# Kernel tuning notes

Measured on AMD Instinct MI355X. Metric: run time of the kernel, lower is better.

Reference implementation:

```python
import jax, jax.numpy as jnp
import numpy as np

B, N, C, H, D = 4, 2048, 512, 8, 64
W = 4            # chunk_window
TOKEEP = 64      # max_keep_keys
NW = N // W      # number of query windows (N divisible by W -> no padding)


def setup_inputs() -> dict:
    key = jax.random.key(0)
    ks = jax.random.split(key, 6)
    x = jax.random.normal(ks[0], (B, N, C), jnp.float32)
    mask = jnp.zeros((B, N), dtype=bool)  # True = padded position
    pos_bias = jax.random.normal(ks[1], (H, N, N), jnp.float32) * 0.02
    # Pareto(scale=3, alpha=2) samples: scale * U^(-1/alpha)
    u = jax.random.uniform(ks[2], (B, H, NW, N), jnp.float32, minval=1e-6, maxval=1.0)
    pareto_noise = 3.0 * u ** (-0.5)
    Wqkv = jax.random.normal(ks[3], (C, 3 * H * D), jnp.float32) * (C ** -0.5)
    bqkv = jnp.zeros((3 * H * D,), jnp.float32)
    Wo = jax.random.normal(ks[4], (H * D, C), jnp.float32) * ((H * D) ** -0.5)
    bo = jnp.zeros((C,), jnp.float32)
    return {"x": x, "mask": mask, "pos_bias": pos_bias, "pareto_noise": pareto_noise,
            "Wqkv": Wqkv, "bqkv": bqkv, "Wo": Wo, "bo": bo}


def reference(x, mask, pos_bias, pareto_noise, Wqkv, bqkv, Wo, bo):
    scale = D ** -0.5
    big = jnp.finfo(x.dtype).max
    # qkv projection; einops '(h d qkv)' => qkv is the innermost factor
    qkv = (x @ Wqkv + bqkv).reshape(B, N, H, D, 3)
    q = qkv[..., 0].transpose(0, 2, 1, 3)  # [B,H,N,D]
    k = qkv[..., 1].transpose(0, 2, 1, 3)
    v = qkv[..., 2].transpose(0, 2, 1, 3)
    q = q.reshape(B, H, NW, W, D)          # windowed queries

    # chunk-distance grid: |chunk_i - chunk_j| repeated W times along keys -> [NW, N]
    ci = jnp.arange(NW)
    grid = jnp.abs(ci[None, :] - ci[:, None]).astype(x.dtype)
    grid = jnp.repeat(grid, W, axis=1)     # [NW, N]
    noised = grid[None, None] - pareto_noise               # [B,H,NW,N]
    noised = jnp.where(mask[:, None, None, :], big, noised)  # padded keys -> never kept

    # keep the TOKEEP smallest (closest, noise-perturbed) keys per window
    _, idx = jax.lax.top_k(-noised, TOKEEP)
    idx = jnp.sort(idx, axis=-1)           # [B,H,NW,K]

    # gather selected keys/values: [B,H,NW,K,D]
    k_sel = jnp.take_along_axis(k[:, :, None], idx[..., None], axis=3)
    v_sel = jnp.take_along_axis(v[:, :, None], idx[..., None], axis=3)

    # position bias gathered at kept keys: [B,H,NW,W,K]
    pb = pos_bias.reshape(H, NW, W, N)[None]
    pb = jnp.take_along_axis(pb, idx[:, :, :, None, :], axis=4)

    dots = jnp.einsum('bhnwd,bhnzd->bhnwz', q, k_sel) * scale + pb

    q_mask = jnp.broadcast_to(mask.reshape(B, 1, NW, W), (B, H, NW, W))
    kv_mask = jnp.take_along_axis(mask[:, None, None, :], idx, axis=3)  # [B,H,NW,K]
    qk = q_mask[..., None] & kv_mask[:, :, :, None, :]  # bool*bool == AND (as in torch code)
    dots = jnp.where(qk, -big, dots)

    attn = jax.nn.softmax(dots, axis=-1)
    out = jnp.einsum('bhnwz,bhnzd->bhnwd', attn, v_sel)   # [B,H,NW,W,D]
    out = out.transpose(0, 2, 3, 1, 4).reshape(B, N, H * D)  # 'b h n w d -> b (n w) (h d)'
    return out @ Wo + bo
```

## Files before the change

kernel.cpp:

```cpp
#include <hip/hip_runtime.h>
#include <stdint.h>

typedef unsigned short u16;
typedef unsigned int u32;
typedef unsigned long long u64;

#define B_ 4
#define N_ 2048
#define C_ 512
#define H_ 8
#define D_ 64
#define W_ 4
#define NW_ 512
#define KEEP_ 64

__device__ __forceinline__ float bf2f(u16 h) { return __uint_as_float(((u32)h) << 16); }
__device__ __forceinline__ u16 f2bf(float f) {
  u32 u = __float_as_uint(f);
  u32 r = (u + 0x7FFFu + ((u >> 16) & 1u)) >> 16;
  return (u16)r;
}
__device__ __forceinline__ u32 flip32(float f) {
  u32 u = __float_as_uint(f);
  return (u & 0x80000000u) ? ~u : (u | 0x80000000u);
}

typedef short bf16x8 __attribute__((ext_vector_type(8)));
typedef float f32x4 __attribute__((ext_vector_type(4)));

__device__ __forceinline__ void async_copy16(u16* lds, const u16* g) {
#if __has_builtin(__builtin_amdgcn_global_load_lds)
  __builtin_amdgcn_global_load_lds((const __attribute__((address_space(1))) u32*)g,
                                   (__attribute__((address_space(3))) u32*)lds, 16, 0, 0);
#else
  const int lane = threadIdx.x & 63;
  *(((uint4*)lds) + lane) = *(const uint4*)g;
#endif
}

__global__ __launch_bounds__(256) void cast_f32_bf16(
    const float* __restrict__ in, u16* __restrict__ out)
{
  const int i = blockIdx.x * 256 + threadIdx.x;
  float4 v = ((const float4*)in)[i];
  uint2 o;
  o.x = (u32)f2bf(v.x) | ((u32)f2bf(v.y) << 16);
  o.y = (u32)f2bf(v.z) | ((u32)f2bf(v.w) << 16);
  ((uint2*)out)[i] = o;
}

__global__ __launch_bounds__(256) void cast_transpose(
    const float* __restrict__ in, u16* __restrict__ out, int R, int C)
{
  __shared__ float tile[64][65];
  const int r0 = blockIdx.y * 64, c0 = blockIdx.x * 64;
  const int tr = threadIdx.x >> 4;
  const int tc = (threadIdx.x & 15) * 4;
#pragma unroll
  for (int i = 0; i < 4; i++) {
    const int r = tr + i * 16;
    float4 v = *(const float4*)(in + (size_t)(r0 + r) * C + c0 + tc);
    tile[r][tc] = v.x; tile[r][tc + 1] = v.y; tile[r][tc + 2] = v.z; tile[r][tc + 3] = v.w;
  }
  __syncthreads();
#pragma unroll
  for (int i = 0; i < 4; i++) {
    const int rr = tr + i * 16;
    uint2 o;
    o.x = (u32)f2bf(tile[tc][rr]) | ((u32)f2bf(tile[tc + 1][rr]) << 16);
    o.y = (u32)f2bf(tile[tc + 2][rr]) | ((u32)f2bf(tile[tc + 3][rr]) << 16);
    *(uint2*)(out + (size_t)(c0 + rr) * R + r0 + tc) = o;
  }
}

template <int MODE>
__global__ __launch_bounds__(256) void gemm_bt(
    const u16* __restrict__ A, const u16* __restrict__ BT, const float* __restrict__ bias,
    void* __restrict__ O0, void* __restrict__ O1, void* __restrict__ O2,
    int M, int N, int K)
{
  __shared__ u16 As[128 * 32];
  __shared__ u16 Bs[128 * 32];
  const int tid = threadIdx.x;
  const int wid = tid >> 6, lane = tid & 63;
  const int tileM = blockIdx.y * 128, tileN = blockIdx.x * 128;
  const int wr = wid >> 1, wc = wid & 1;

  f32x4 acc[4][4];
#pragma unroll
  for (int i = 0; i < 4; i++)
#pragma unroll
    for (int j = 0; j < 4; j++) acc[i][j] = (f32x4){0.f, 0.f, 0.f, 0.f};

  const int srow = wid * 32 + (lane >> 2);
  const int scol = (lane & 3) * 8;
  const u16* Ag = A + (size_t)(tileM + srow) * K + scol;
  const u16* Bg = BT + (size_t)(tileN + srow) * K + scol;
  u16* AsW = As + wid * 32 * 32;
  u16* BsW = Bs + wid * 32 * 32;

  const int fr = lane & 15, fq = lane >> 4;

  for (int k0 = 0; k0 < K; k0 += 32) {
    __syncthreads();
    async_copy16(AsW, Ag + k0);
    async_copy16(AsW + 16 * 32, Ag + k0 + (size_t)16 * K);
    async_copy16(BsW, Bg + k0);
    async_copy16(BsW + 16 * 32, Bg + k0 + (size_t)16 * K);
    asm volatile("s_waitcnt vmcnt(0)" ::: "memory");
    __syncthreads();

    bf16x8 af[4], bfr[4];
#pragma unroll
    for (int tm = 0; tm < 4; tm++)
      af[tm] = *(const bf16x8*)(As + (wr * 64 + tm * 16 + fr) * 32 + fq * 8);
#pragma unroll
    for (int tn = 0; tn < 4; tn++)
      bfr[tn] = *(const bf16x8*)(Bs + (wc * 64 + tn * 16 + fr) * 32 + fq * 8);
#pragma unroll
    for (int tm = 0; tm < 4; tm++)
#pragma unroll
      for (int tn = 0; tn < 4; tn++)
        acc[tm][tn] = __builtin_amdgcn_mfma_f32_16x16x32_bf16(af[tm], bfr[tn], acc[tm][tn], 0, 0, 0);
  }

#pragma unroll
  for (int tm = 0; tm < 4; tm++) {
#pragma unroll
    for (int tn = 0; tn < 4; tn++) {
      const int colb = tileN + wc * 64 + tn * 16 + fr;
      const float bi = bias[colb];
      if (MODE == 0) {
        const int h = colb / 192;
        const int rem = colb - h * 192;
        const int d = rem / 3;
        const int tq = rem - d * 3;
        u16* dst = (tq == 0) ? (u16*)O0 : (tq == 1) ? (u16*)O1 : (u16*)O2;
#pragma unroll
        for (int r = 0; r < 4; r++) {
          const int row = tileM + wr * 64 + tm * 16 + fq * 4 + r;
          const int b = row >> 11, n = row & 2047;
          const size_t off = (((size_t)(b * 8 + h)) * 2048 + n) * 64 + d;
          dst[off] = f2bf(acc[tm][tn][r] + bi);
        }
      } else {
        float* Of = (float*)O0;
#pragma unroll
        for (int r = 0; r < 4; r++) {
          const int row = tileM + wr * 64 + tm * 16 + fq * 4 + r;
          Of[(size_t)row * N + colb] = acc[tm][tn][r] + bi;
        }
      }
    }
  }
}

__global__ __launch_bounds__(256) void select_topk(
    const float* __restrict__ noise, u16* __restrict__ idx_out)
{
  const int wid = threadIdx.x >> 6;
  const int lane = threadIdx.x & 63;
  const int pid = blockIdx.x * 4 + wid;
  const int nw = pid & (NW_ - 1);

  __shared__ u64 pool_s[4][512];
  u64* pool = pool_s[wid];

  const int s = min(nw, (NW_ - 1) - nw);
  const float T = (s >= 8) ? 5.0f : (float)(12 - s);

  const float* row = noise + (size_t)pid * N_;
  float4 f[8];
#pragma unroll
  for (int k = 0; k < 8; k++)
    f[k] = *(const float4*)(row + k * 256 + lane * 4);

  const u64 lmask = (1ull << lane) - 1ull;
  u32 c = 0;
#pragma unroll
  for (int k = 0; k < 8; k++) {
    const int ci = k * 64 + lane;
    const int dd = nw - ci;
    const float g = (float)(dd < 0 ? -dd : dd);
    const float vv[4] = {f[k].x, f[k].y, f[k].z, f[k].w};
#pragma unroll
    for (int e = 0; e < 4; e++) {
      const float v = g - vv[e];
      const bool sv = (v <= T);
      const u64 mask = __ballot(sv);
      if (sv) {
        const u32 pos = c + (u32)__popcll(mask & lmask);
        const int j = k * 256 + lane * 4 + e;
        if (pos < 512) pool[pos] = ((u64)flip32(v) << 16) | (u32)j;
      }
      c += (u32)__popcll(mask);
    }
  }
  __syncthreads();

  u16* outp = idx_out + (size_t)pid * KEEP_;

  if (__builtin_expect(c > 512, 0)) {
    u32 taken = 0;
    u16 keep = 0;
    for (int r = 0; r < 64; r++) {
      u64 best = ~0ull;
      int bslot = -1;
#pragma unroll
      for (int k = 0; k < 8; k++) {
        const int ci = k * 64 + lane;
        const int dd = nw - ci;
        const float g = (float)(dd < 0 ? -dd : dd);
        const float vv[4] = {f[k].x, f[k].y, f[k].z, f[k].w};
#pragma unroll
        for (int e = 0; e < 4; e++) {
          const int sl = k * 4 + e;
          if (!(taken & (1u << sl))) {
            const int j = k * 256 + lane * 4 + e;
            const u64 p = ((u64)flip32(g - vv[e]) << 16) | (u32)j;
            if (p < best) { best = p; bslot = sl; }
          }
        }
      }
      u64 m = best;
#pragma unroll
      for (int st = 1; st < 64; st <<= 1) {
        const u64 o = __shfl_xor(m, st, 64);
        if (o < m) m = o;
      }
      if (best == m) taken |= (1u << bslot);
      if (lane == r) keep = (u16)(m & 0xFFFFu);
    }
    outp[lane] = keep;
    return;
  }

  u64 q[8];
#pragma unroll
  for (int k = 0; k < 8; k++) {
    const u32 sl = (u32)lane + (u32)(k << 6);
    q[k] = (sl < c) ? pool[sl] : 0ull;
  }
  int cnt = ((u32)lane < c) ? (int)((c - 1 - (u32)lane) >> 6) + 1 : 0;

#define CE_(a, b) { if (q[a] < q[b]) { u64 t_ = q[a]; q[a] = q[b]; q[b] = t_; } }
  CE_(0,1) CE_(2,3) CE_(4,5) CE_(6,7)
  CE_(0,2) CE_(1,3) CE_(4,6) CE_(5,7)
  CE_(1,2) CE_(5,6)
  CE_(0,4) CE_(1,5) CE_(2,6) CE_(3,7)
  CE_(2,4) CE_(3,5)
  CE_(1,2) CE_(3,4) CE_(5,6)
#undef CE_

  const int R = (int)c - KEEP_;
  for (int r = 0; r < R; r++) {
    u64 m = q[0];
#pragma unroll
    for (int st = 1; st < 64; st <<= 1) {
      const u64 o = __shfl_xor(m, st, 64);
      if (o > m) m = o;
    }
    if (q[0] == m) {
      q[0] = q[1]; q[1] = q[2]; q[2] = q[3]; q[3] = q[4];
      q[4] = q[5]; q[5] = q[6]; q[6] = q[7]; q[7] = 0ull;
      cnt--;
    }
  }

  u32 off = (u32)cnt;
#pragma unroll
  for (int st = 1; st < 64; st <<= 1) {
    const u32 o = __shfl_up(off, st, 64);
    if (lane >= st) off += o;
  }
  off -= (u32)cnt;
#pragma unroll
  for (int k = 0; k < 8; k++)
    if (k < cnt) outp[off + k] = (u16)(q[k] & 0xFFFFu);
}

__global__ __launch_bounds__(256) void attn_kernel(
    const u16* __restrict__ Q, const u16* __restrict__ Kt, const u16* __restrict__ Vt,
    const float* __restrict__ pos_bias, const u16* __restrict__ idx, u16* __restrict__ outp)
{
  const int bid = blockIdx.x;
  const int b = bid & 3;
  const int hn = bid >> 2;
  const int h = hn >> 9;
  const int nw = hn & (NW_ - 1);
  const int bh = b * H_ + h;
  const int pid = bh * NW_ + nw;
  const int t = threadIdx.x;

  __shared__ float q_s[W_][D_];
  __shared__ u16 k_s[64 * 66];
  __shared__ u16 v_s[64 * 66];
  __shared__ float attn_s[W_][64];
  __shared__ u16 idx_s[64];

  if (t < 64) {
    idx_s[t] = idx[(size_t)pid * KEEP_ + t];
    const int w = t >> 4, dq = (t & 15) * 4;
    uint2 v = *(const uint2*)(Q + ((size_t)bh * N_ + nw * W_ + w) * D_ + dq);
    q_s[w][dq] = bf2f((u16)(v.x & 0xFFFF));
    q_s[w][dq + 1] = bf2f((u16)(v.x >> 16));
    q_s[w][dq + 2] = bf2f((u16)(v.y & 0xFFFF));
    q_s[w][dq + 3] = bf2f((u16)(v.y >> 16));
  }
  __syncthreads();

  const int w2 = t >> 6, z2 = t & 63;
  float pb;
  {
    const int z = t >> 2, c = t & 3;
    const u32 kidx = idx_s[z];
    const u16* kr = Kt + ((size_t)bh * N_ + kidx) * D_ + c * 16;
    const u16* vr = Vt + ((size_t)bh * N_ + kidx) * D_ + c * 16;
    uint4 ka = *(const uint4*)kr;
    uint4 kb = *(const uint4*)(kr + 8);
    uint4 va = *(const uint4*)vr;
    uint4 vb = *(const uint4*)(vr + 8);
    u32* kd = (u32*)(k_s + z * 66 + c * 16);
    u32* vd = (u32*)(v_s + z * 66 + c * 16);
    kd[0] = ka.x; kd[1] = ka.y; kd[2] = ka.z; kd[3] = ka.w;
    kd[4] = kb.x; kd[5] = kb.y; kd[6] = kb.z; kd[7] = kb.w;
    vd[0] = va.x; vd[1] = va.y; vd[2] = va.z; vd[3] = va.w;
    vd[4] = vb.x; vd[5] = vb.y; vd[6] = vb.z; vd[7] = vb.w;
    pb = pos_bias[((size_t)h * N_ + nw * W_ + w2) * N_ + idx_s[z2]];
  }
  __syncthreads();

  float accd = 0.f;
  const u16* krow = k_s + z2 * 66;
#pragma unroll
  for (int d = 0; d < 64; d += 2) {
    u32 pr = *(const u32*)(krow + d);
    accd += q_s[w2][d] * bf2f((u16)(pr & 0xFFFF));
    accd += q_s[w2][d + 1] * bf2f((u16)(pr >> 16));
  }
  float dots = accd * 0.125f + pb;

  float m = dots;
#pragma unroll
  for (int off = 1; off < 64; off <<= 1) m = fmaxf(m, __shfl_xor(m, off, 64));
  float e = __expf(dots - m);
  float sden = e;
#pragma unroll
  for (int off = 1; off < 64; off <<= 1) sden += __shfl_xor(sden, off, 64);
  attn_s[w2][z2] = e / sden;
  __syncthreads();

  const int d3 = t & 63;
  float o = 0.f;
#pragma unroll
  for (int z = 0; z < 64; z++) o += attn_s[w2][z] * bf2f(v_s[z * 66 + d3]);
  outp[((size_t)b * N_ + nw * W_ + w2) * (H_ * D_) + h * D_ + d3] = f2bf(o);
}

extern "C" void kernel_launch(void* const* d_in, const int* in_sizes, int n_in,
                              void* d_out, int out_size, void* d_ws, size_t ws_size,
                              hipStream_t stream)
{
  const float* x = (const float*)d_in[0];
  const float* pos_bias = (const float*)d_in[2];
  const float* pareto = (const float*)d_in[3];
  const float* Wqkv = (const float*)d_in[4];
  const float* bqkv = (const float*)d_in[5];
  const float* Wo = (const float*)d_in[6];
  const float* bo = (const float*)d_in[7];
  float* out = (float*)d_out;

  char* w = (char*)d_ws;
  u16* xb = (u16*)w;    w += (size_t)8192 * 512 * 2;
  u16* WqkvT = (u16*)w; w += (size_t)1536 * 512 * 2;
  u16* WoT = (u16*)w;   w += (size_t)512 * 512 * 2;
  u16* Qb = (u16*)w;    w += (size_t)B_ * H_ * N_ * D_ * 2;
  u16* Kb = (u16*)w;    w += (size_t)B_ * H_ * N_ * D_ * 2;
  u16* Vb = (u16*)w;    w += (size_t)B_ * H_ * N_ * D_ * 2;
  u16* idxb = (u16*)w;  w += (size_t)B_ * H_ * NW_ * KEEP_ * 2;
  u16* attn_o = (u16*)w;

  cast_f32_bf16<<<(8192 * 512) / 1024, 256, 0, stream>>>(x, xb);
  cast_transpose<<<dim3(1536 / 64, 512 / 64), 256, 0, stream>>>(Wqkv, WqkvT, 512, 1536);
  cast_transpose<<<dim3(512 / 64, 512 / 64), 256, 0, stream>>>(Wo, WoT, 512, 512);
  gemm_bt<0><<<dim3(1536 / 128, 8192 / 128), 256, 0, stream>>>(
      xb, WqkvT, bqkv, Qb, Kb, Vb, 8192, 1536, 512);
  select_topk<<<(B_ * H_ * NW_) / 4, 256, 0, stream>>>(pareto, idxb);
  attn_kernel<<<B_ * H_ * NW_, 256, 0, stream>>>(Qb, Kb, Vb, pos_bias, idxb, attn_o);
  gemm_bt<1><<<dim3(512 / 128, 8192 / 128), 256, 0, stream>>>(
      attn_o, WoT, bo, out, nullptr, nullptr, 8192, 512, 512);
}
```

Baseline: 426.9 us.

## Replace ballot compaction and iterative max-removal with prefix-sum compaction and rank selection

The candidate pool is now filled by having each lane build a bitmask of survivors, taking a wave-wide prefix sum once, and writing its entries contiguously. This replaces a ballot and popcount per element. The top-k step drops the per-lane sorting network and the loop that removed the current maximum with a shuffle reduction once per excess element. Instead, each lane counts how many pool entries are smaller than each of its candidates and writes the entry directly to its rank slot when the rank is below KEEP. This cuts the serial shuffle-reduction rounds, but every lane now scans the whole pool through shared memory, which costs O(c) LDS reads.

```diff
diff --git a/kernel.cpp b/kernel.cpp
--- a/kernel.cpp
+++ b/kernel.cpp
@@ -175,8 +175,7 @@
   for (int k = 0; k < 8; k++)
     f[k] = *(const float4*)(row + k * 256 + lane * 4);
 
-  const u64 lmask = (1ull << lane) - 1ull;
-  u32 c = 0;
+  u32 smask = 0;
 #pragma unroll
   for (int k = 0; k < 8; k++) {
     const int ci = k * 64 + lane;
@@ -184,16 +183,35 @@
     const float g = (float)(dd < 0 ? -dd : dd);
     const float vv[4] = {f[k].x, f[k].y, f[k].z, f[k].w};
 #pragma unroll
-    for (int e = 0; e < 4; e++) {
-      const float v = g - vv[e];
-      const bool sv = (v <= T);
-      const u64 mask = __ballot(sv);
-      if (sv) {
-        const u32 pos = c + (u32)__popcll(mask & lmask);
-        const int j = k * 256 + lane * 4 + e;
-        if (pos < 512) pool[pos] = ((u64)flip32(v) << 16) | (u32)j;
+    for (int e = 0; e < 4; e++)
+      if (g - vv[e] <= T) smask |= (1u << (k * 4 + e));
+  }
+  const u32 scnt = (u32)__popc(smask);
+
+  u32 pre = scnt;
+#pragma unroll
+  for (int st = 1; st < 64; st <<= 1) {
+    const u32 o = __shfl_up(pre, st, 64);
+    if (lane >= st) pre += o;
+  }
+  const u32 c = __shfl(pre, 63, 64);
+  u32 wo = pre - scnt;
+
+  if (smask && c <= 512) {
+#pragma unroll
+    for (int k = 0; k < 8; k++) {
+      if (!(smask >> (k * 4))) continue;
+      const int ci = k * 64 + lane;
+      const int dd = nw - ci;
+      const float g = (float)(dd < 0 ? -dd : dd);
+      const float vv[4] = {f[k].x, f[k].y, f[k].z, f[k].w};
+#pragma unroll
+      for (int e = 0; e < 4; e++) {
+        if (smask & (1u << (k * 4 + e))) {
+          const int j = k * 256 + lane * 4 + e;
+          pool[wo++] = ((u64)flip32(g - vv[e]) << 16) | (u32)j;
+        }
       }
-      c += (u32)__popcll(mask);
     }
   }
   __syncthreads();
@@ -235,48 +253,26 @@
     return;
   }
 
-  u64 q[8];
+  const int nm = ((u32)lane < c) ? (int)((c - 1 - (u32)lane) >> 6) + 1 : 0;
+  u64 mine[8];
+  u32 rank[8];
 #pragma unroll
   for (int k = 0; k < 8; k++) {
-    const u32 sl = (u32)lane + (u32)(k << 6);
-    q[k] = (sl < c) ? pool[sl] : 0ull;
-  }
-  int cnt = ((u32)lane < c) ? (int)((c - 1 - (u32)lane) >> 6) + 1 : 0;
-
-#define CE_(a, b) { if (q[a] < q[b]) { u64 t_ = q[a]; q[a] = q[b]; q[b] = t_; } }
-  CE_(0,1) CE_(2,3) CE_(4,5) CE_(6,7)
-  CE_(0,2) CE_(1,3) CE_(4,6) CE_(5,7)
-  CE_(1,2) CE_(5,6)
-  CE_(0,4) CE_(1,5) CE_(2,6) CE_(3,7)
-  CE_(2,4) CE_(3,5)
-  CE_(1,2) CE_(3,4) CE_(5,6)
-#undef CE_
-
-  const int R = (int)c - KEEP_;
-  for (int r = 0; r < R; r++) {
-    u64 m = q[0];
-#pragma unroll
-    for (int st = 1; st < 64; st <<= 1) {
-      const u64 o = __shfl_xor(m, st, 64);
-      if (o > m) m = o;
-    }
-    if (q[0] == m) {
-      q[0] = q[1]; q[1] = q[2]; q[2] = q[3]; q[3] = q[4];
-      q[4] = q[5]; q[5] = q[6]; q[6] = q[7]; q[7] = 0ull;
-      cnt--;
-    }
-  }
-
-  u32 off = (u32)cnt;
-#pragma unroll
-  for (int st = 1; st < 64; st <<= 1) {
-    const u32 o = __shfl_up(off, st, 64);
-    if (lane >= st) off += o;
-  }
-  off -= (u32)cnt;
+    mine[k] = (k < nm) ? pool[lane + (k << 6)] : ~0ull;
+    rank[k] = 0;
+  }
+#pragma unroll 4
+  for (u32 i = 0; i < c; i++) {
+    const u64 p = pool[i];
+#pragma unroll
+    for (int k = 0; k < 2; k++) rank[k] += (p < mine[k]) ? 1u : 0u;
+    if (nm > 2)
+#pragma unroll
+      for (int k = 2; k < 8; k++) rank[k] += (p < mine[k]) ? 1u : 0u;
+  }
 #pragma unroll
   for (int k = 0; k < 8; k++)
-    if (k < cnt) outp[off + k] = (u16)(q[k] & 0xFFFFu);
+    if (k < nm && rank[k] < KEEP_) outp[rank[k]] = (u16)(mine[k] & 0xFFFFu);
 }
 
 __global__ __launch_bounds__(256) void attn_kernel(
```

Measured after the change: 383.6 us. 10.1% less time.
